# Optimization experiments

Measured on AMD Instinct MI355X. Metric: run time of the kernel, lower is better.

The kernel has to match this reference:

```python
import jax, jax.numpy as jnp
import numpy as np

K = 10  # neighbor_num from init_kwargs


def setup_inputs() -> dict:
    key = jax.random.key(0)
    k1, k2 = jax.random.split(key)
    xyz = jax.random.normal(k1, (8, 16384, 3), dtype=jnp.float32)
    sample_xyz = jax.random.normal(k2, (8, 1024, 3), dtype=jnp.float32)
    temp = jnp.ones((), dtype=jnp.float32)  # init_temp = 1.0
    return {"xyz": xyz, "sample_xyz": sample_xyz, "temp": temp}


def reference(xyz, sample_xyz, temp):
    # Pairwise squared distances [B, S, N] via ||a-b||^2 = ||a||^2 + ||b||^2 - 2 a.b
    q2 = jnp.sum(sample_xyz * sample_xyz, axis=-1)            # [B, S]
    p2 = jnp.sum(xyz * xyz, axis=-1)                          # [B, N]
    cross = jnp.einsum('bsd,bnd->bsn', sample_xyz, xyz)       # [B, S, N]
    d2 = q2[:, :, None] + p2[:, None, :] - 2.0 * cross
    d2 = jnp.maximum(d2, 0.0)
    # K nearest neighbors (smallest squared distance)
    neg_top, idx = jax.lax.top_k(-d2, K)                      # [B, S, K]
    squared_dist = -neg_top
    # Gather neighbor coordinates: [B, S, K, 3]
    neighbor_xyz = jax.vmap(lambda pts, ids: pts[ids])(xyz, idx)
    # Softmax weights over the K neighbors
    weight = jax.nn.softmax(-squared_dist / (temp * temp), axis=-1)  # [B, S, K]
    proj_xyz = jnp.sum(neighbor_xyz * weight[..., None], axis=-2)    # [B, S, 3]
    return (proj_xyz, temp)
```

## Files before the change

kernel.cpp:

```cpp
#include <hip/hip_runtime.h>
#include <math.h>

#define NPTS 16384
#define NSMP 8192
#define KNN 10
#define QPB 8
#define WAVES 8
#define SLICE 2048
#define GPW 16
#define CAP 96

typedef float v2f __attribute__((ext_vector_type(2)));
typedef unsigned long long u64;

__device__ __forceinline__ unsigned mapf(float f) {
    unsigned u = __float_as_uint(f);
    return (u & 0x80000000u) ? ~u : (u | 0x80000000u);
}
__device__ __forceinline__ float unmapf(unsigned k) {
    unsigned u = (k & 0x80000000u) ? (k ^ 0x80000000u) : ~k;
    return __uint_as_float(u);
}
__device__ __forceinline__ float uniform_f(float x) {
    return __uint_as_float(__builtin_amdgcn_readfirstlane(__float_as_uint(x)));
}

__global__ __launch_bounds__(256) void pack_kernel(const float* __restrict__ xyz,
                                                   float4* __restrict__ pk) {
    const int t = blockIdx.x * 256 + threadIdx.x;
    const int b = t >> 13;
    const int r = t & 8191;
    const int g = r >> 6;
    const int l = r & 63;
    const float* pA = xyz + ((size_t)b * NPTS + (size_t)g * 128 + l) * 3;
    const float* pB = pA + 64 * 3;
    const float xA = pA[0], yA = pA[1], zA = pA[2];
    const float xB = pB[0], yB = pB[1], zB = pB[2];
    const float wA = fmaf(xA, xA, fmaf(yA, yA, zA * zA));
    const float wB = fmaf(xB, xB, fmaf(yB, yB, zB * zB));
    float4* dst = pk + ((size_t)(b * 128 + g) * 128);
    dst[l]      = make_float4(xA, xB, yA, yB);
    dst[l + 64] = make_float4(zA, zB, wA, wB);
}

__global__ __launch_bounds__(512, 4) void knn_kernel(
    const float4* __restrict__ pk,
    const float* __restrict__ xyz,
    const float* __restrict__ sxyz,
    const float* __restrict__ temp,
    float* __restrict__ out)
{
    __shared__ float minBuf[QPB][WAVES * 64];
    __shared__ unsigned tauU[QPB];
    __shared__ int   cnt[QPB];
    __shared__ u64   candK[QPB][CAP];
    __shared__ u64   sort10[QPB][KNN];

    const int lane  = threadIdx.x & 63;
    const int w     = threadIdx.x >> 6;
    const int qbase = blockIdx.x * QPB;
    const int b     = qbase >> 10;

    if (threadIdx.x < QPB) cnt[threadIdx.x] = 0;

    float ax[QPB], ay[QPB], az[QPB];
    #pragma unroll
    for (int q = 0; q < QPB; ++q) {
        const float* s = sxyz + (size_t)(qbase + q) * 3;
        ax[q] = uniform_f(-2.f * s[0]);
        ay[q] = uniform_f(-2.f * s[1]);
        az[q] = uniform_f(-2.f * s[2]);
    }

    const float4* pw = pk + ((size_t)(b * 128 + w * 16)) * 128 + lane;
    const int sbase = w * SLICE;

    v2f mn[QPB];
    #pragma unroll
    for (int q = 0; q < QPB; ++q) { mn[q].x = INFINITY; mn[q].y = INFINITY; }

    #pragma unroll 2
    for (int j = 0; j < GPW; ++j) {
        const float4 c0 = pw[(size_t)j * 128];
        const float4 c1 = pw[(size_t)j * 128 + 64];
        const v2f X = {c0.x, c0.y}, Y = {c0.z, c0.w};
        const v2f Z = {c1.x, c1.y}, W = {c1.z, c1.w};
        #pragma unroll
        for (int q = 0; q < QPB; ++q) {
            const v2f d = X * ax[q] + (Y * ay[q] + (Z * az[q] + W));
            mn[q] = __builtin_elementwise_min(mn[q], d);
        }
    }
    #pragma unroll
    for (int q = 0; q < QPB; ++q) minBuf[q][w * 64 + lane] = fminf(mn[q].x, mn[q].y);
    __syncthreads();

    {
        float vm = minBuf[w][lane];
        #pragma unroll
        for (int k = 1; k < WAVES; ++k) vm = fminf(vm, minBuf[w][k * 64 + lane]);
        const unsigned um = mapf(vm);
        unsigned lo = 0u, hi = 0xFFFFFFFFu;
        #pragma unroll 1
        for (int it = 0; it < 16; ++it) {
            const unsigned mid = lo + ((hi - lo) >> 1);
            const int c = __popcll(__ballot(um <= mid));
            if (c >= KNN) hi = mid; else lo = mid + 1;
        }
        if (lane == 0) tauU[w] = hi;
    }
    __syncthreads();

    float tau[QPB];
    #pragma unroll
    for (int q = 0; q < QPB; ++q) tau[q] = uniform_f(unmapf(tauU[q]));

    #pragma unroll 1
    for (int j = 0; j < GPW; ++j) {
        const float4 c0 = pw[(size_t)j * 128];
        const float4 c1 = pw[(size_t)j * 128 + 64];
        const v2f X = {c0.x, c0.y}, Y = {c0.z, c0.w};
        const v2f Z = {c1.x, c1.y}, W = {c1.z, c1.w};
        const int idx0 = sbase + j * 128 + lane;
        #pragma unroll
        for (int q = 0; q < QPB; ++q) {
            const float tq = tau[q];
            const v2f d = X * ax[q] + (Y * ay[q] + (Z * az[q] + W));
            if (__ballot(fminf(d.x, d.y) <= tq)) {
                if (d.x <= tq) { const int s = atomicAdd(&cnt[q], 1);
                    if (s < CAP) candK[q][s] = ((u64)mapf(d.x) << 32) | (unsigned)idx0; }
                if (d.y <= tq) { const int s = atomicAdd(&cnt[q], 1);
                    if (s < CAP) candK[q][s] = ((u64)mapf(d.y) << 32) | (unsigned)(idx0 + 64); }
            }
        }
    }
    __syncthreads();

    {
        const int q   = w;
        const int gid = qbase + q;
        const int c   = min(cnt[q], CAP);

        const u64 k0 = (lane      < c) ? candK[q][lane]      : ~0ull;
        const u64 k1 = (lane + 64 < c) ? candK[q][lane + 64] : ~0ull;
        int r0 = 0, r1 = 0;
        for (int jj = 0; jj < c; ++jj) {
            const u64 kj = candK[q][jj];
            r0 += (kj < k0) ? 1 : 0;
            r1 += (kj < k1) ? 1 : 0;
        }
        if (lane      < c && r0 < KNN) sort10[q][r0] = k0;
        if (lane + 64 < c && r1 < KNN) sort10[q][r1] = k1;
        const u64 sel = (lane < KNN) ? sort10[q][lane] : ~0ull;

        const float* s = sxyz + (size_t)gid * 3;
        const float q2 = fmaf(s[0], s[0], fmaf(s[1], s[1], s[2] * s[2]));
        const float dp = unmapf((unsigned)(sel >> 32));
        const float d2v = fmaxf(dp + q2, 0.f);
        const float dmin = __shfl(d2v, 0);
        const float t = temp[0];
        const float invt2 = 1.0f / (t * t);
        float wgt = 0.f, px = 0.f, py = 0.f, pz = 0.f;
        if (lane < KNN) {
            wgt = __expf((dmin - d2v) * invt2);
            const int idx = (int)(unsigned)(sel & 0xFFFFFFFFull);
            const float* pp = xyz + ((size_t)b * NPTS + idx) * 3;
            px = pp[0]; py = pp[1]; pz = pp[2];
        }
        float sw = wgt, sx = wgt * px, sy = wgt * py, sz = wgt * pz;
        #pragma unroll
        for (int off = 8; off >= 1; off >>= 1) {
            sw += __shfl_xor(sw, off);
            sx += __shfl_xor(sx, off);
            sy += __shfl_xor(sy, off);
            sz += __shfl_xor(sz, off);
        }
        if (lane == 0) {
            const float inv = 1.0f / sw;
            out[(size_t)gid * 3 + 0] = sx * inv;
            out[(size_t)gid * 3 + 1] = sy * inv;
            out[(size_t)gid * 3 + 2] = sz * inv;
            if (gid == 0) out[NSMP * 3] = t;
        }
    }
}

extern "C" void kernel_launch(void* const* d_in, const int* in_sizes, int n_in,
                              void* d_out, int out_size, void* d_ws, size_t ws_size,
                              hipStream_t stream) {
    const float* xyz  = (const float*)d_in[0];
    const float* sxyz = (const float*)d_in[1];
    const float* temp = (const float*)d_in[2];
    float* out = (float*)d_out;

    float4* pk = (float4*)d_ws;

    hipLaunchKernelGGL(pack_kernel, dim3(256), dim3(256), 0, stream, xyz, pk);
    hipLaunchKernelGGL(knn_kernel, dim3(NSMP / QPB), dim3(512), 0, stream,
                       pk, xyz, sxyz, temp, out);
}
```

Before: 47.80 us.

## Rescan only lane-groups whose minimum beats threshold instead of full second pass

New measurement: 42.37 us. 11.4% less time.

```diff
diff --git a/kernel.cpp b/kernel.cpp
--- a/kernel.cpp
+++ b/kernel.cpp
@@ -8,7 +8,8 @@
 #define WAVES 8
 #define SLICE 2048
 #define GPW 16
-#define CAP 96
+#define CAP 64
+#define LCAP 160
 
 typedef float v2f __attribute__((ext_vector_type(2)));
 typedef unsigned long long u64;
@@ -26,7 +27,8 @@
 }
 
 __global__ __launch_bounds__(256) void pack_kernel(const float* __restrict__ xyz,
-                                                   float4* __restrict__ pk) {
+                                                   float4* __restrict__ pk,
+                                                   float4* __restrict__ pk2) {
     const int t = blockIdx.x * 256 + threadIdx.x;
     const int b = t >> 13;
     const int r = t & 8191;
@@ -41,18 +43,21 @@
     float4* dst = pk + ((size_t)(b * 128 + g) * 128);
     dst[l]      = make_float4(xA, xB, yA, yB);
     dst[l + 64] = make_float4(zA, zB, wA, wB);
+    float4* dst2 = pk2 + (size_t)b * NPTS + (size_t)g * 128;
+    dst2[l]      = make_float4(xA, yA, zA, wA);
+    dst2[l + 64] = make_float4(xB, yB, zB, wB);
 }
 
 __global__ __launch_bounds__(512, 4) void knn_kernel(
     const float4* __restrict__ pk,
-    const float* __restrict__ xyz,
+    const float4* __restrict__ pk2,
     const float* __restrict__ sxyz,
     const float* __restrict__ temp,
     float* __restrict__ out)
 {
     __shared__ float minBuf[QPB][WAVES * 64];
-    __shared__ unsigned tauU[QPB];
     __shared__ int   cnt[QPB];
+    __shared__ int   list[QPB][LCAP];
     __shared__ u64   candK[QPB][CAP];
     __shared__ u64   sort10[QPB][KNN];
 
@@ -73,7 +78,6 @@
     }
 
     const float4* pw = pk + ((size_t)(b * 128 + w * 16)) * 128 + lane;
-    const int sbase = w * SLICE;
 
     v2f mn[QPB];
     #pragma unroll
@@ -95,66 +99,63 @@
     for (int q = 0; q < QPB; ++q) minBuf[q][w * 64 + lane] = fminf(mn[q].x, mn[q].y);
     __syncthreads();
 
+    const int gid = qbase + w;
+    const float* sq = sxyz + (size_t)gid * 3;
+    const float bx = -2.f * sq[0], by = -2.f * sq[1], bz = -2.f * sq[2];
+
+    float mi[WAVES];
+    #pragma unroll
+    for (int k = 0; k < WAVES; ++k) mi[k] = minBuf[w][k * 64 + lane];
+    float vm = mi[0];
+    #pragma unroll
+    for (int k = 1; k < WAVES; ++k) vm = fminf(vm, mi[k]);
+    const unsigned um = mapf(vm);
+    unsigned lo = 0u, hi = 0xFFFFFFFFu;
+    #pragma unroll 1
+    for (int it = 0; it < 16; ++it) {
+        const unsigned mid = lo + ((hi - lo) >> 1);
+        const int c = __popcll(__ballot(um <= mid));
+        if (c >= KNN) hi = mid; else lo = mid + 1;
+    }
+    const float tau = unmapf(hi);
+
+    int nf = 0;
+    #pragma unroll
+    for (int k = 0; k < WAVES; ++k) {
+        const bool flg = (mi[k] <= tau);
+        const u64 m = __ballot(flg);
+        const int pos = nf + __popcll(m & ((1ull << lane) - 1ull));
+        if (flg && pos < LCAP) list[w][pos] = k * 64 + lane;
+        nf += __popcll(m);
+    }
+    if (nf > LCAP) nf = LCAP;
+
+    const float4* p2 = pk2 + (size_t)b * NPTS;
+    const int total = nf * 32;
+    for (int i = lane; i < total; i += 64) {
+        const int sid = list[w][i >> 5];
+        const int p   = i & 31;
+        const int idx = ((sid >> 6) << 11) + ((p >> 1) << 7) + ((p & 1) << 6) + (sid & 63);
+        const float4 pt = p2[idx];
+        const float d = fmaf(pt.x, bx, fmaf(pt.y, by, fmaf(pt.z, bz, pt.w)));
+        if (d <= tau) {
+            const int s = atomicAdd(&cnt[w], 1);
+            if (s < CAP) candK[w][s] = ((u64)mapf(d) << 32) | (unsigned)idx;
+        }
+    }
+
     {
-        float vm = minBuf[w][lane];
-        #pragma unroll
-        for (int k = 1; k < WAVES; ++k) vm = fminf(vm, minBuf[w][k * 64 + lane]);
-        const unsigned um = mapf(vm);
-        unsigned lo = 0u, hi = 0xFFFFFFFFu;
-        #pragma unroll 1
-        for (int it = 0; it < 16; ++it) {
-            const unsigned mid = lo + ((hi - lo) >> 1);
-            const int c = __popcll(__ballot(um <= mid));
-            if (c >= KNN) hi = mid; else lo = mid + 1;
-        }
-        if (lane == 0) tauU[w] = hi;
-    }
-    __syncthreads();
-
-    float tau[QPB];
-    #pragma unroll
-    for (int q = 0; q < QPB; ++q) tau[q] = uniform_f(unmapf(tauU[q]));
-
-    #pragma unroll 1
-    for (int j = 0; j < GPW; ++j) {
-        const float4 c0 = pw[(size_t)j * 128];
-        const float4 c1 = pw[(size_t)j * 128 + 64];
-        const v2f X = {c0.x, c0.y}, Y = {c0.z, c0.w};
-        const v2f Z = {c1.x, c1.y}, W = {c1.z, c1.w};
-        const int idx0 = sbase + j * 128 + lane;
-        #pragma unroll
-        for (int q = 0; q < QPB; ++q) {
-            const float tq = tau[q];
-            const v2f d = X * ax[q] + (Y * ay[q] + (Z * az[q] + W));
-            if (__ballot(fminf(d.x, d.y) <= tq)) {
-                if (d.x <= tq) { const int s = atomicAdd(&cnt[q], 1);
-                    if (s < CAP) candK[q][s] = ((u64)mapf(d.x) << 32) | (unsigned)idx0; }
-                if (d.y <= tq) { const int s = atomicAdd(&cnt[q], 1);
-                    if (s < CAP) candK[q][s] = ((u64)mapf(d.y) << 32) | (unsigned)(idx0 + 64); }
-            }
-        }
-    }
-    __syncthreads();
-
-    {
-        const int q   = w;
-        const int gid = qbase + q;
-        const int c   = min(cnt[q], CAP);
-
-        const u64 k0 = (lane      < c) ? candK[q][lane]      : ~0ull;
-        const u64 k1 = (lane + 64 < c) ? candK[q][lane + 64] : ~0ull;
-        int r0 = 0, r1 = 0;
+        const int c = min(cnt[w], CAP);
+        const u64 k0 = (lane < c) ? candK[w][lane] : ~0ull;
+        int r0 = 0;
         for (int jj = 0; jj < c; ++jj) {
-            const u64 kj = candK[q][jj];
+            const u64 kj = candK[w][jj];
             r0 += (kj < k0) ? 1 : 0;
-            r1 += (kj < k1) ? 1 : 0;
-        }
-        if (lane      < c && r0 < KNN) sort10[q][r0] = k0;
-        if (lane + 64 < c && r1 < KNN) sort10[q][r1] = k1;
-        const u64 sel = (lane < KNN) ? sort10[q][lane] : ~0ull;
-
-        const float* s = sxyz + (size_t)gid * 3;
-        const float q2 = fmaf(s[0], s[0], fmaf(s[1], s[1], s[2] * s[2]));
+        }
+        if (lane < c && r0 < KNN) sort10[w][r0] = k0;
+        const u64 sel = (lane < KNN) ? sort10[w][lane] : ~0ull;
+
+        const float q2 = fmaf(sq[0], sq[0], fmaf(sq[1], sq[1], sq[2] * sq[2]));
         const float dp = unmapf((unsigned)(sel >> 32));
         const float d2v = fmaxf(dp + q2, 0.f);
         const float dmin = __shfl(d2v, 0);
@@ -164,8 +165,8 @@
         if (lane < KNN) {
             wgt = __expf((dmin - d2v) * invt2);
             const int idx = (int)(unsigned)(sel & 0xFFFFFFFFull);
-            const float* pp = xyz + ((size_t)b * NPTS + idx) * 3;
-            px = pp[0]; py = pp[1]; pz = pp[2];
+            const float4 pp = p2[idx];
+            px = pp.x; py = pp.y; pz = pp.z;
         }
         float sw = wgt, sx = wgt * px, sy = wgt * py, sz = wgt * pz;
         #pragma unroll
@@ -193,9 +194,10 @@
     const float* temp = (const float*)d_in[2];
     float* out = (float*)d_out;
 
-    float4* pk = (float4*)d_ws;
-
-    hipLaunchKernelGGL(pack_kernel, dim3(256), dim3(256), 0, stream, xyz, pk);
+    float4* pk  = (float4*)d_ws;
+    float4* pk2 = (float4*)((char*)d_ws + (size_t)131072*16);
+
+    hipLaunchKernelGGL(pack_kernel, dim3(256), dim3(256), 0, stream, xyz, pk, pk2);
     hipLaunchKernelGGL(knn_kernel, dim3(NSMP / QPB), dim3(512), 0, stream,
-                       pk, xyz, sxyz, temp, out);
-}
+                       pk, pk2, sxyz, temp, out);
+}
```
